# Kernel optimization log

Hardware: AMD Instinct MI355X
Metric: run time of the kernel (lower is better)

The kernel has to match this reference:

```python
import jax, jax.numpy as jnp
import numpy as np

VOCAB, D, L, LT, B = 50000, 300, 256, 8, 256
N_HOPS, N_CLASSES = 6, 3
NEG_INF = -1e9


def setup_inputs() -> dict:
    key = jax.random.key(0)
    ks = jax.random.split(key, 12)
    s = 0.05
    return {
        "embeddings": jax.random.normal(ks[0], (VOCAB, D), jnp.float32) * s,
        "w_lin": jax.random.normal(ks[1], (D, D), jnp.float32) * s,
        "b_lin": jax.random.normal(ks[2], (D,), jnp.float32) * s,
        "w_att": jax.random.normal(ks[3], (2 * D,), jnp.float32) * s,
        "b_att": jax.random.normal(ks[4], (), jnp.float32) * s,
        "w_out": jax.random.normal(ks[5], (D, N_CLASSES), jnp.float32) * s,
        "b_out": jax.random.normal(ks[6], (N_CLASSES,), jnp.float32) * s,
        "context_ids": jax.random.randint(ks[7], (B, L), 0, VOCAB, jnp.int32),
        "context_len": jax.random.randint(ks[8], (B,), 1, L + 1, jnp.int32),
        "target_ids": jax.random.randint(ks[9], (B, LT), 0, VOCAB, jnp.int32),
        "target_len": jax.random.randint(ks[10], (B,), 1, LT + 1, jnp.int32),
        "target_loc": jax.random.randint(ks[11], (B,), 0, L, jnp.int32),
    }


def reference(embeddings, w_lin, b_lin, w_att, b_att, w_out, b_out,
              context_ids, context_len, target_ids, target_len, target_loc):
    # context memory: [B, L, D]
    m = embeddings[context_ids]
    pos = jnp.arange(L)
    mask = pos[None, :] < context_len[:, None]                     # [B, L]
    lens = context_len.astype(jnp.float32)[:, None]
    # absolute distance location vector (model 2): v_i = 1 - |i - loc| / len
    dist = jnp.abs(pos[None, :] - target_loc[:, None]).astype(jnp.float32)
    v_loc = jnp.where(mask, 1.0 - dist / lens, 0.0)                # [B, L]
    ext_mem = m * v_loc[:, :, None]                                # [B, L, D]

    # aspect vector: masked mean of target embeddings -> [B, D]
    tgt = embeddings[target_ids]                                   # [B, LT, D]
    tmask = (jnp.arange(LT)[None, :] < target_len[:, None]).astype(jnp.float32)
    v_aspect = jnp.einsum("btd,bt->bd", tgt, tmask) / target_len.astype(jnp.float32)[:, None]

    vec = v_aspect
    for _ in range(N_HOPS):  # shared weights across hops (AUTO_REUSE)
        linear_out = vec @ w_lin + b_lin                           # [B, D]
        # content attention: score_i = tanh(w_att . [m_i ; v] + b)
        scores = (jnp.einsum("bld,d->bl", ext_mem, w_att[:D])
                  + (vec @ w_att[D:])[:, None] + b_att)
        scores = jnp.tanh(scores)
        alpha = jax.nn.softmax(jnp.where(mask, scores, NEG_INF), axis=-1)
        attn_out = jnp.einsum("bl,bld->bd", alpha, ext_mem)
        vec = attn_out + linear_out

    logits = vec @ w_out + b_out                                   # [B, C]
    return logits
```

## Files before the change

### kernel.cpp

```cpp
#include <hip/hip_runtime.h>

typedef unsigned short u16;
typedef unsigned int   u32;
typedef __fp16 h2t __attribute__((ext_vector_type(2)));

#define D      300
#define L      256
#define LT     8
#define B      256
#define NHOPS  6
#define NCLS   3
#define NT     1024
#define NKP    156

#define OFF_E    0
#define OFF_VEC  153600
#define OFF_VPK  154848
#define OFF_APK  155472
#define OFF_S0   155984
#define OFF_CTX  157008
#define SMEM_BYTES 158032

#define DPP_ADD(x, ctrl) \
    x += __int_as_float(__builtin_amdgcn_update_dpp(0, __float_as_int(x), ctrl, 0xf, 0xf, true))

__device__ __forceinline__ float dpp_wave_sum(float x) {
    DPP_ADD(x, 0x111);
    DPP_ADD(x, 0x112);
    DPP_ADD(x, 0x114);
    DPP_ADD(x, 0x118);
    DPP_ADD(x, 0x142);
    DPP_ADD(x, 0x143);
    return x;
}
__device__ __forceinline__ float lane63(float x) {
    return __int_as_float(__builtin_amdgcn_readlane(__float_as_int(x), 63));
}
__device__ __forceinline__ u32 pk16(float a, float b) {
    h2t r = __builtin_amdgcn_cvt_pkrtz(a, b);
    return __builtin_bit_cast(u32, r);
}
__device__ __forceinline__ float fdot2(u32 a, u32 b, float c) {
    return __builtin_amdgcn_fdot2(__builtin_bit_cast(h2t, a),
                                  __builtin_bit_cast(h2t, b), c, false);
}

__launch_bounds__(NT, 1)
__global__ void cvt_wpk(const float* __restrict__ w, u32* __restrict__ o) {
    int idx = blockIdx.x * NT + threadIdx.x;
    if (idx < NKP * D) {
        int kp = idx / D, col = idx - kp * D;
        int k0 = 2 * kp;
        float a = (k0     < D) ? w[k0 * D + col]       : 0.f;
        float b = (k0 + 1 < D) ? w[(k0 + 1) * D + col] : 0.f;
        o[idx] = pk16(a, b);
    }
}

template<int WPK>
__launch_bounds__(NT, 1)
__global__ void memnet_main(
    const float* __restrict__ emb,
    const float* __restrict__ w_lin,
    const u32*  __restrict__ wpk,
    const float* __restrict__ b_lin,
    const float* __restrict__ w_att,
    const float* __restrict__ b_att,
    const float* __restrict__ w_out,
    const float* __restrict__ b_out,
    const int* __restrict__ ctx_ids,
    const int* __restrict__ ctx_len,
    const int* __restrict__ tgt_ids,
    const int* __restrict__ tgt_len,
    const int* __restrict__ tgt_loc,
    float* __restrict__ out)
{
    extern __shared__ char sm[];
    float* vec_ = (float*)(sm + OFF_VEC);
    u32*   vpk_ = (u32*)(sm + OFF_VPK);
    u32*   apk_ = (u32*)(sm + OFF_APK);
    float* s0_  = (float*)(sm + OFF_S0);
    int*   ctx_ = (int*)(sm + OFF_CTX);

    const int b = blockIdx.x, t = threadIdx.x;
    const int lane = t & 63, wv = t >> 6;
    const int c  = lane / 5;
    const int qi = lane - 5 * c;
    const int q  = 5 * wv + qi;
    const bool heavy = (wv < 15) && (lane < 60);

    const int clen = ctx_len[b], tlen = tgt_len[b], loc = tgt_loc[b];
    const int lps  = (clen + 1) >> 1;

    if (t < L) { ctx_[t] = ctx_ids[b * L + t]; s0_[t] = 0.f; }
    if (t >= 300 && t < 312) vec_[t] = 0.f;
    if (t < 6) vpk_[150 + t] = 0;
    __syncthreads();

    {
        const float4 z4 = make_float4(0.f, 0.f, 0.f, 0.f);
        float4 wa1 = ((const float4*)w_att)[lane];
        float4 wa2 = z4;
        if (lane < 11) wa2 = ((const float4*)w_att)[64 + lane];
        const float rclen = 1.f / (float)clen;
        for (int lp = wv; lp < lps; lp += 16) {
            const int l0 = 2 * lp, l1 = l0 + 1;
            const float4* e0 = (const float4*)(emb + (long)ctx_[l0] * D);
            const float4* e1 = (const float4*)(emb + (long)ctx_[l1] * D);
            const float4 a0 = e0[lane];
            const float4 a1 = e1[lane];
            float4 b0 = z4, b1 = z4;
            if (lane < 11) { b0 = e0[64 + lane]; b1 = e1[64 + lane]; }
            float d0 = a0.x*wa1.x + a0.y*wa1.y + a0.z*wa1.z + a0.w*wa1.w
                     + b0.x*wa2.x + b0.y*wa2.y + b0.z*wa2.z + b0.w*wa2.w;
            float d1 = a1.x*wa1.x + a1.y*wa1.y + a1.z*wa1.z + a1.w*wa1.w
                     + b1.x*wa2.x + b1.y*wa2.y + b1.z*wa2.z + b1.w*wa2.w;
            d0 = dpp_wave_sum(d0);
            d1 = dpp_wave_sum(d1);
            const float vl0 = 1.f - fabsf((float)(l0 - loc)) * rclen;
            const float vl1 = (l1 < clen) ? 1.f - fabsf((float)(l1 - loc)) * rclen : 0.f;
            if (lane == 63) { s0_[l0] = vl0 * d0; s0_[l1] = vl1 * d1; }
            uint4 P;
            P.x = pk16(a0.x * vl0, a1.x * vl1);
            P.y = pk16(a0.y * vl0, a1.y * vl1);
            P.z = pk16(a0.z * vl0, a1.z * vl1);
            P.w = pk16(a0.w * vl0, a1.w * vl1);
            *(uint4*)(sm + OFF_E + (lp * 300 + 4 * lane) * 4) = P;
            if (lane < 11) {
                uint4 Q;
                Q.x = pk16(b0.x * vl0, b1.x * vl1);
                Q.y = pk16(b0.y * vl0, b1.y * vl1);
                Q.z = pk16(b0.z * vl0, b1.z * vl1);
                Q.w = pk16(b0.w * vl0, b1.w * vl1);
                *(uint4*)(sm + OFF_E + (lp * 300 + 256 + 4 * lane) * 4) = Q;
            }
        }
    }

    if (t < D) {
        float s = 0.f;
        for (int j = 0; j < tlen; ++j)
            s += emb[(long)tgt_ids[b * LT + j] * D + t];
        const float v = s / (float)tlen;
        vec_[t] = v;
        const float v2 = __shfl_xor(v, 1);
        if ((t & 1) == 0) vpk_[t >> 1] = pk16(v, v2);
    }

    uint4 wreg[13];
    if (WPK && heavy) {
        #pragma unroll
        for (int i = 0; i < 13; ++i)
            wreg[i] = *(const uint4*)(wpk + (13 * c + i) * 300 + 4 * q);
    }
    const float4 z4 = make_float4(0.f, 0.f, 0.f, 0.f);
    float4 blin4 = z4;
    if (heavy) blin4 = *(const float4*)(b_lin + 4 * q);
    __syncthreads();

    float4 s0r = z4, wb1 = z4, wb2 = z4;
    float batt = 0.f;
    if (wv == 15) {
        s0r = *(const float4*)(s0_ + 4 * lane);
        wb1 = *(const float4*)(w_att + D + 4 * lane);
        if (lane < 11) wb2 = *(const float4*)(w_att + D + 256 + 4 * lane);
        batt = b_att[0];
    }

    for (int hop = 0; hop < NHOPS; ++hop) {
        float4 acc = z4;
        if (heavy) {
            const u32* vp = vpk_ + 13 * c;
            #pragma unroll
            for (int i = 0; i < 13; ++i) {
                const u32 v2 = vp[i];
                if (WPK) {
                    const uint4 w4 = wreg[i];
                    acc.x = fdot2(v2, w4.x, acc.x);
                    acc.y = fdot2(v2, w4.y, acc.y);
                    acc.z = fdot2(v2, w4.z, acc.z);
                    acc.w = fdot2(v2, w4.w, acc.w);
                } else {
                    const int k0 = 26 * c + 2 * i;
                    const float4 w0 = (k0     < D) ? *(const float4*)(w_lin + (long)k0 * D + 4 * q) : z4;
                    const float4 w1 = (k0 + 1 < D) ? *(const float4*)(w_lin + (long)(k0 + 1) * D + 4 * q) : z4;
                    const float v0 = vec_[k0], v1 = vec_[k0 + 1];
                    acc.x += v0 * w0.x + v1 * w1.x;
                    acc.y += v0 * w0.y + v1 * w1.y;
                    acc.z += v0 * w0.z + v1 * w1.z;
                    acc.w += v0 * w0.w + v1 * w1.w;
                }
            }
        } else if (wv == 15) {
            const float4 v1 = *(const float4*)(vec_ + 4 * lane);
            float4 v2 = z4;
            if (lane < 11) v2 = *(const float4*)(vec_ + 256 + 4 * lane);
            float p = v1.x*wb1.x + v1.y*wb1.y + v1.z*wb1.z + v1.w*wb1.w
                    + v2.x*wb2.x + v2.y*wb2.y + v2.z*wb2.z + v2.w*wb2.w;
            p = dpp_wave_sum(p);
            const float tb = lane63(p) + batt;
            const int lb = 4 * lane;
            float e0 = 0.f, e1 = 0.f, e2 = 0.f, e3 = 0.f;
            {
                float x, E2, th;
                x = s0r.x + tb; E2 = __expf(2.f * x);
                th = 1.f - 2.f * __builtin_amdgcn_rcpf(E2 + 1.f);
                if (lb + 0 < clen) e0 = __expf(th);
                x = s0r.y + tb; E2 = __expf(2.f * x);
                th = 1.f - 2.f * __builtin_amdgcn_rcpf(E2 + 1.f);
                if (lb + 1 < clen) e1 = __expf(th);
                x = s0r.z + tb; E2 = __expf(2.f * x);
                th = 1.f - 2.f * __builtin_amdgcn_rcpf(E2 + 1.f);
                if (lb + 2 < clen) e2 = __expf(th);
                x = s0r.w + tb; E2 = __expf(2.f * x);
                th = 1.f - 2.f * __builtin_amdgcn_rcpf(E2 + 1.f);
                if (lb + 3 < clen) e3 = __expf(th);
            }
            float es = dpp_wave_sum(e0 + e1 + e2 + e3);
            const float rinv = __builtin_amdgcn_rcpf(lane63(es));
            *(uint2*)(sm + OFF_APK + 8 * lane) =
                make_uint2(pk16(e0 * rinv, e1 * rinv), pk16(e2 * rinv, e3 * rinv));
        }
        __syncthreads();

        if (heavy) {
            const int lp0 = 11 * c;
            const u32* ap = apk_ + lp0;
            const char* ep = sm + OFF_E + (lp0 * 300 + 4 * q) * 4;
            #pragma unroll
            for (int r = 0; r < 11; ++r) {
                if (lp0 + r < lps) {
                    const u32 av2 = ap[r];
                    const uint4 e4 = *(const uint4*)(ep + r * 1200);
                    acc.x = fdot2(av2, e4.x, acc.x);
                    acc.y = fdot2(av2, e4.y, acc.y);
                    acc.z = fdot2(av2, e4.z, acc.z);
                    acc.w = fdot2(av2, e4.w, acc.w);
                }
            }
            float4 s;
            s.x = __shfl(acc.x, lane + 30); s.y = __shfl(acc.y, lane + 30);
            s.z = __shfl(acc.z, lane + 30); s.w = __shfl(acc.w, lane + 30);
            if (c < 6) { acc.x += s.x; acc.y += s.y; acc.z += s.z; acc.w += s.w; }
            s.x = __shfl(acc.x, lane + 15); s.y = __shfl(acc.y, lane + 15);
            s.z = __shfl(acc.z, lane + 15); s.w = __shfl(acc.w, lane + 15);
            if (c < 3) { acc.x += s.x; acc.y += s.y; acc.z += s.z; acc.w += s.w; }
            float4 u1, u2;
            u1.x = __shfl(acc.x, lane + 5);  u1.y = __shfl(acc.y, lane + 5);
            u1.z = __shfl(acc.z, lane + 5);  u1.w = __shfl(acc.w, lane + 5);
            u2.x = __shfl(acc.x, lane + 10); u2.y = __shfl(acc.y, lane + 10);
            u2.z = __shfl(acc.z, lane + 10); u2.w = __shfl(acc.w, lane + 10);
            if (c == 0) {
                float4 nv;
                nv.x = acc.x + u1.x + u2.x + blin4.x;
                nv.y = acc.y + u1.y + u2.y + blin4.y;
                nv.z = acc.z + u1.z + u2.z + blin4.z;
                nv.w = acc.w + u1.w + u2.w + blin4.w;
                *(float4*)(vec_ + 4 * q) = nv;
                *(uint2*)(sm + OFF_VPK + 8 * q) =
                    make_uint2(pk16(nv.x, nv.y), pk16(nv.z, nv.w));
            }
        }
        __syncthreads();
    }

    if (wv < NCLS) {
        float p = 0.f;
        for (int i = lane; i < D; i += 64)
            p += vec_[i] * w_out[i * NCLS + wv];
        p = dpp_wave_sum(p);
        if (lane == 63) out[b * NCLS + wv] = p + b_out[wv];
    }
}

extern "C" void kernel_launch(void* const* d_in, const int* in_sizes, int n_in,
                              void* d_out, int out_size, void* d_ws, size_t ws_size,
                              hipStream_t stream) {
    const float* emb     = (const float*)d_in[0];
    const float* w_lin   = (const float*)d_in[1];
    const float* b_lin   = (const float*)d_in[2];
    const float* w_att   = (const float*)d_in[3];
    const float* b_att   = (const float*)d_in[4];
    const float* w_out   = (const float*)d_in[5];
    const float* b_out   = (const float*)d_in[6];
    const int*   ctx_ids = (const int*)d_in[7];
    const int*   ctx_len = (const int*)d_in[8];
    const int*   tgt_ids = (const int*)d_in[9];
    const int*   tgt_len = (const int*)d_in[10];
    const int*   tgt_loc = (const int*)d_in[11];
    float* out = (float*)d_out;

    const size_t WBYTES = (size_t)NKP * D * sizeof(u32);
    if (ws_size >= WBYTES) {
        u32* wpk = (u32*)d_ws;
        cvt_wpk<<<(NKP * D + NT - 1) / NT, NT, 0, stream>>>(w_lin, wpk);
        (void)hipFuncSetAttribute((const void*)memnet_main<1>,
                                  hipFuncAttributeMaxDynamicSharedMemorySize,
                                  SMEM_BYTES);
        memnet_main<1><<<B, NT, SMEM_BYTES, stream>>>(
            emb, w_lin, wpk, b_lin, w_att, b_att, w_out, b_out,
            ctx_ids, ctx_len, tgt_ids, tgt_len, tgt_loc, out);
    } else {
        (void)hipFuncSetAttribute((const void*)memnet_main<0>,
                                  hipFuncAttributeMaxDynamicSharedMemorySize,
                                  SMEM_BYTES);
        memnet_main<0><<<B, NT, SMEM_BYTES, stream>>>(
            emb, w_lin, (const u32*)nullptr, b_lin, w_att, b_att, w_out, b_out,
            ctx_ids, ctx_len, tgt_ids, tgt_len, tgt_loc, out);
    }
}
```

Before: 36.25 us.

## Fold w_lin fp16 packing into main kernel and vectorize LDS operand reads

```diff
diff --git a/kernel.cpp b/kernel.cpp
--- a/kernel.cpp
+++ b/kernel.cpp
@@ -11,15 +11,14 @@
 #define NHOPS  6
 #define NCLS   3
 #define NT     1024
-#define NKP    156
 
 #define OFF_E    0
 #define OFF_VEC  153600
 #define OFF_VPK  154848
-#define OFF_APK  155472
-#define OFF_S0   155984
-#define OFF_CTX  157008
-#define SMEM_BYTES 158032
+#define OFF_APK  155808
+#define OFF_S0   156384
+#define OFF_CTX  157408
+#define SMEM_BYTES 158432
 
 #define DPP_ADD(x, ctrl) \
     x += __int_as_float(__builtin_amdgcn_update_dpp(0, __float_as_int(x), ctrl, 0xf, 0xf, true))
@@ -46,23 +45,9 @@
 }
 
 __launch_bounds__(NT, 1)
-__global__ void cvt_wpk(const float* __restrict__ w, u32* __restrict__ o) {
-    int idx = blockIdx.x * NT + threadIdx.x;
-    if (idx < NKP * D) {
-        int kp = idx / D, col = idx - kp * D;
-        int k0 = 2 * kp;
-        float a = (k0     < D) ? w[k0 * D + col]       : 0.f;
-        float b = (k0 + 1 < D) ? w[(k0 + 1) * D + col] : 0.f;
-        o[idx] = pk16(a, b);
-    }
-}
-
-template<int WPK>
-__launch_bounds__(NT, 1)
 __global__ void memnet_main(
     const float* __restrict__ emb,
     const float* __restrict__ w_lin,
-    const u32*  __restrict__ wpk,
     const float* __restrict__ b_lin,
     const float* __restrict__ w_att,
     const float* __restrict__ b_att,
@@ -92,13 +77,29 @@
     const int clen = ctx_len[b], tlen = tgt_len[b], loc = tgt_loc[b];
     const int lps  = (clen + 1) >> 1;
 
+    const float4 z4 = make_float4(0.f, 0.f, 0.f, 0.f);
+
     if (t < L) { ctx_[t] = ctx_ids[b * L + t]; s0_[t] = 0.f; }
     if (t >= 300 && t < 312) vec_[t] = 0.f;
-    if (t < 6) vpk_[150 + t] = 0;
+    if (t >= 768 && t < 1008) vpk_[t - 768] = 0;
     __syncthreads();
 
+    uint4 wreg[13];
+    if (heavy) {
+        #pragma unroll
+        for (int i = 0; i < 13; ++i) {
+            const int k0 = 26 * c + 2 * i;
+            float4 w0 = z4, w1 = z4;
+            if (k0 < D)     w0 = *(const float4*)(w_lin + (long)k0 * D + 4 * q);
+            if (k0 + 1 < D) w1 = *(const float4*)(w_lin + (long)(k0 + 1) * D + 4 * q);
+            wreg[i].x = pk16(w0.x, w1.x);
+            wreg[i].y = pk16(w0.y, w1.y);
+            wreg[i].z = pk16(w0.z, w1.z);
+            wreg[i].w = pk16(w0.w, w1.w);
+        }
+    }
+
     {
-        const float4 z4 = make_float4(0.f, 0.f, 0.f, 0.f);
         float4 wa1 = ((const float4*)w_att)[lane];
         float4 wa2 = z4;
         if (lane < 11) wa2 = ((const float4*)w_att)[64 + lane];
@@ -138,22 +139,26 @@
     }
 
     if (t < D) {
+        int ids[LT];
+        #pragma unroll
+        for (int j = 0; j < LT; ++j) ids[j] = tgt_ids[b * LT + j];
         float s = 0.f;
-        for (int j = 0; j < tlen; ++j)
-            s += emb[(long)tgt_ids[b * LT + j] * D + t];
+        #pragma unroll
+        for (int j = 0; j < LT; ++j) {
+            const int  safe = (j < tlen) ? ids[j] : ids[0];
+            const float msk = (j < tlen) ? 1.f : 0.f;
+            s += msk * emb[(long)safe * D + t];
+        }
         const float v = s / (float)tlen;
         vec_[t] = v;
         const float v2 = __shfl_xor(v, 1);
-        if ((t & 1) == 0) vpk_[t >> 1] = pk16(v, v2);
-    }
-
-    uint4 wreg[13];
-    if (WPK && heavy) {
-        #pragma unroll
-        for (int i = 0; i < 13; ++i)
-            wreg[i] = *(const uint4*)(wpk + (13 * c + i) * 300 + 4 * q);
-    }
-    const float4 z4 = make_float4(0.f, 0.f, 0.f, 0.f);
+        if ((t & 1) == 0) {
+            const int kp = t >> 1;
+            const int cp = kp / 13, sl = kp - 13 * cp;
+            vpk_[20 * cp + sl] = pk16(v, v2);
+        }
+    }
+
     float4 blin4 = z4;
     if (heavy) blin4 = *(const float4*)(b_lin + 4 * q);
     __syncthreads();
@@ -170,28 +175,20 @@
     for (int hop = 0; hop < NHOPS; ++hop) {
         float4 acc = z4;
         if (heavy) {
-            const u32* vp = vpk_ + 13 * c;
+            const uint4* vp4 = (const uint4*)(vpk_ + 20 * c);
+            const uint4 V0 = vp4[0], V1 = vp4[1], V2 = vp4[2], V3 = vp4[3];
+            const u32 vs[13] = {V0.x, V0.y, V0.z, V0.w,
+                                V1.x, V1.y, V1.z, V1.w,
+                                V2.x, V2.y, V2.z, V2.w, V3.x};
             #pragma unroll
             for (int i = 0; i < 13; ++i) {
-                const u32 v2 = vp[i];
-                if (WPK) {
-                    const uint4 w4 = wreg[i];
-                    acc.x = fdot2(v2, w4.x, acc.x);
-                    acc.y = fdot2(v2, w4.y, acc.y);
-                    acc.z = fdot2(v2, w4.z, acc.z);
-                    acc.w = fdot2(v2, w4.w, acc.w);
-                } else {
-                    const int k0 = 26 * c + 2 * i;
-                    const float4 w0 = (k0     < D) ? *(const float4*)(w_lin + (long)k0 * D + 4 * q) : z4;
-                    const float4 w1 = (k0 + 1 < D) ? *(const float4*)(w_lin + (long)(k0 + 1) * D + 4 * q) : z4;
-                    const float v0 = vec_[k0], v1 = vec_[k0 + 1];
-                    acc.x += v0 * w0.x + v1 * w1.x;
-                    acc.y += v0 * w0.y + v1 * w1.y;
-                    acc.z += v0 * w0.z + v1 * w1.z;
-                    acc.w += v0 * w0.w + v1 * w1.w;
-                }
+                acc.x = fdot2(vs[i], wreg[i].x, acc.x);
+                acc.y = fdot2(vs[i], wreg[i].y, acc.y);
+                acc.z = fdot2(vs[i], wreg[i].z, acc.z);
+                acc.w = fdot2(vs[i], wreg[i].w, acc.w);
             }
         } else if (wv == 15) {
+            __builtin_amdgcn_s_setprio(1);
             const float4 v1 = *(const float4*)(vec_ + 4 * lane);
             float4 v2 = z4;
             if (lane < 11) v2 = *(const float4*)(vec_ + 256 + 4 * lane);
@@ -218,24 +215,31 @@
             }
             float es = dpp_wave_sum(e0 + e1 + e2 + e3);
             const float rinv = __builtin_amdgcn_rcpf(lane63(es));
-            *(uint2*)(sm + OFF_APK + 8 * lane) =
-                make_uint2(pk16(e0 * rinv, e1 * rinv), pk16(e2 * rinv, e3 * rinv));
+            const int p0 = 2 * lane, p1 = p0 + 1;
+            const int c0 = p0 / 11, sl0 = p0 - 11 * c0;
+            const int c1 = p1 / 11, sl1 = p1 - 11 * c1;
+            apk_[12 * c0 + sl0] = pk16(e0 * rinv, e1 * rinv);
+            apk_[12 * c1 + sl1] = pk16(e2 * rinv, e3 * rinv);
+            __builtin_amdgcn_s_setprio(0);
         }
         __syncthreads();
 
         if (heavy) {
+            const uint4* ap4 = (const uint4*)(apk_ + 12 * c);
+            const uint4 A0 = ap4[0], A1 = ap4[1], A2 = ap4[2];
+            const u32 as[12] = {A0.x, A0.y, A0.z, A0.w,
+                                A1.x, A1.y, A1.z, A1.w,
+                                A2.x, A2.y, A2.z, A2.w};
             const int lp0 = 11 * c;
-            const u32* ap = apk_ + lp0;
             const char* ep = sm + OFF_E + (lp0 * 300 + 4 * q) * 4;
             #pragma unroll
             for (int r = 0; r < 11; ++r) {
                 if (lp0 + r < lps) {
-                    const u32 av2 = ap[r];
                     const uint4 e4 = *(const uint4*)(ep + r * 1200);
-                    acc.x = fdot2(av2, e4.x, acc.x);
-                    acc.y = fdot2(av2, e4.y, acc.y);
-                    acc.z = fdot2(av2, e4.z, acc.z);
-                    acc.w = fdot2(av2, e4.w, acc.w);
+                    acc.x = fdot2(as[r], e4.x, acc.x);
+                    acc.y = fdot2(as[r], e4.y, acc.y);
+                    acc.z = fdot2(as[r], e4.z, acc.z);
+                    acc.w = fdot2(as[r], e4.w, acc.w);
                 }
             }
             float4 s;
@@ -257,8 +261,11 @@
                 nv.z = acc.z + u1.z + u2.z + blin4.z;
                 nv.w = acc.w + u1.w + u2.w + blin4.w;
                 *(float4*)(vec_ + 4 * q) = nv;
-                *(uint2*)(sm + OFF_VPK + 8 * q) =
-                    make_uint2(pk16(nv.x, nv.y), pk16(nv.z, nv.w));
+                const int p0 = 2 * q, p1 = p0 + 1;
+                const int ca = p0 / 13, sa = p0 - 13 * ca;
+                const int cb = p1 / 13, sb = p1 - 13 * cb;
+                vpk_[20 * ca + sa] = pk16(nv.x, nv.y);
+                vpk_[20 * cb + sb] = pk16(nv.z, nv.w);
             }
         }
         __syncthreads();
@@ -290,22 +297,10 @@
     const int*   tgt_loc = (const int*)d_in[11];
     float* out = (float*)d_out;
 
-    const size_t WBYTES = (size_t)NKP * D * sizeof(u32);
-    if (ws_size >= WBYTES) {
-        u32* wpk = (u32*)d_ws;
-        cvt_wpk<<<(NKP * D + NT - 1) / NT, NT, 0, stream>>>(w_lin, wpk);
-        (void)hipFuncSetAttribute((const void*)memnet_main<1>,
-                                  hipFuncAttributeMaxDynamicSharedMemorySize,
-                                  SMEM_BYTES);
-        memnet_main<1><<<B, NT, SMEM_BYTES, stream>>>(
-            emb, w_lin, wpk, b_lin, w_att, b_att, w_out, b_out,
-            ctx_ids, ctx_len, tgt_ids, tgt_len, tgt_loc, out);
-    } else {
-        (void)hipFuncSetAttribute((const void*)memnet_main<0>,
-                                  hipFuncAttributeMaxDynamicSharedMemorySize,
-                                  SMEM_BYTES);
-        memnet_main<0><<<B, NT, SMEM_BYTES, stream>>>(
-            emb, w_lin, (const u32*)nullptr, b_lin, w_att, b_att, w_out, b_out,
-            ctx_ids, ctx_len, tgt_ids, tgt_len, tgt_loc, out);
-    }
-}
+    (void)hipFuncSetAttribute((const void*)memnet_main,
+                              hipFuncAttributeMaxDynamicSharedMemorySize,
+                              SMEM_BYTES);
+    memnet_main<<<B, NT, SMEM_BYTES, stream>>>(
+        emb, w_lin, b_lin, w_att, b_att, w_out, b_out,
+        ctx_ids, ctx_len, tgt_ids, tgt_len, tgt_loc, out);
+}
```

Measured after the change: 34.05 us. -6.1%, faster.
